# Optimization experiments

Measured on AMD Instinct MI355X. Metric: run time of the kernel, lower is better.

Reference implementation:

```python
import jax, jax.numpy as jnp
import numpy as np

B, N, NP, K, C_IN, C, H = 16, 4096, 1024, 32, 128, 256, 4
C_G = C_IN + 3  # grouped feature dim (use_xyz concat of relative coords)
EPS = 1e-3      # keras LayerNormalization default epsilon


def setup_inputs() -> dict:
    key = jax.random.key(0)
    ks = jax.random.split(key, 16)
    s = 0.05
    return {
        "xyz": jax.random.normal(ks[0], (B, N, 3), jnp.float32),
        "newxyz": jax.random.normal(ks[1], (B, NP, 3), jnp.float32),
        "feature_input": jax.random.normal(ks[2], (B, N, C_IN), jnp.float32),
        "w_qkv": jax.random.normal(ks[3], (C_G, 3 * C), jnp.float32) * s,
        "proj_w": jax.random.normal(ks[4], (C, C), jnp.float32) * s,
        "proj_b": jnp.zeros((C,), jnp.float32),
        "dense_w": jax.random.normal(ks[5], (C_G, C), jnp.float32) * s,
        "dense_b": jnp.zeros((C,), jnp.float32),
        "fc1_w": jax.random.normal(ks[6], (C, 2 * C), jnp.float32) * s,
        "fc1_b": jnp.zeros((2 * C,), jnp.float32),
        "fc2_w": jax.random.normal(ks[7], (2 * C, C), jnp.float32) * s,
        "fc2_b": jnp.zeros((C,), jnp.float32),
        "n1_g": jnp.ones((C_G,), jnp.float32),
        "n1_b": jnp.zeros((C_G,), jnp.float32),
        "n2_g": jnp.ones((C,), jnp.float32),
        "n2_b": jnp.zeros((C,), jnp.float32),
        "group_num": K,
        "training": True,
    }


def _layernorm(x, g, b):
    m = jnp.mean(x, axis=-1, keepdims=True)
    v = jnp.mean(jnp.square(x - m), axis=-1, keepdims=True)
    return (x - m) * jax.lax.rsqrt(v + EPS) * g + b


def _sample_and_group(newxyz, group_num, xyz, feats):
    # squared pairwise distances (B, NP, N)
    d2 = (jnp.sum(newxyz**2, -1)[:, :, None]
          - 2.0 * jnp.einsum('bpc,bnc->bpn', newxyz, xyz)
          + jnp.sum(xyz**2, -1)[:, None, :])
    _, idx = jax.lax.top_k(-d2, group_num)            # (B, NP, K) nearest
    b_idx = jnp.arange(newxyz.shape[0])[:, None, None]
    grouped_xyz = xyz[b_idx, idx] - newxyz[:, :, None, :]   # (B, NP, K, 3)
    grouped_feat = feats[b_idx, idx]                        # (B, NP, K, C_IN)
    return jnp.concatenate([grouped_xyz, grouped_feat], axis=-1)


def _self_attention(x, w_qkv, proj_w, proj_b):
    b, n, k = x.shape[0], x.shape[1], x.shape[2]
    d = C // H
    qkv = jnp.einsum('bnkc,cd->bnkd', x, w_qkv)
    qkv = qkv.reshape(b, n, k, 3, H, d)
    qkv = jnp.transpose(qkv, (3, 0, 1, 4, 2, 5))      # (3, B, NP, H, K, d)
    q, kk, v = qkv[0], qkv[1], qkv[2]
    qm = jnp.max(q, axis=-2, keepdims=True)           # (B, NP, H, 1, d)
    attn = jnp.einsum('bnhqd,bnhkd->bnhqk', qm, kk) * (C ** -0.5)
    attn = jax.nn.softmax(attn, axis=-1)
    out = jnp.einsum('bnhqk,bnhkd->bnhqd', attn, v)[..., 0, :]  # (B, NP, H, d)
    out = out.reshape(b, n, C)
    return jax.nn.relu(out @ proj_w + proj_b)


def reference(xyz, newxyz, feature_input, w_qkv, proj_w, proj_b, dense_w,
              dense_b, fc1_w, fc1_b, fc2_w, fc2_b, n1_g, n1_b, n2_g, n2_b,
              group_num, training):
    gf = _sample_and_group(newxyz, group_num, xyz, feature_input)  # (B,NP,K,C_G)
    feat = _self_attention(_layernorm(gf, n1_g, n1_b), w_qkv, proj_w, proj_b)
    feat = feat + jax.nn.relu(jnp.max(gf, axis=-2) @ dense_w + dense_b)
    f2 = _layernorm(feat, n2_g, n2_b)
    f2 = jax.nn.relu(f2 @ fc1_w + fc1_b)
    f2 = f2 @ fc2_w + fc2_b
    return f2 + feat
```

## Files before the change

kernel.cpp:

```cpp
#include <hip/hip_runtime.h>
#include <hip/hip_bf16.h>

typedef __hip_bfloat16 bf16;

#define Bn   16
#define Nn   4096
#define NPn  1024
#define Kn   32
#define CINn 128
#define CGn  131
#define Cn   256
#define Hn   4
#define KPAD 160
#define XBS  168
#define XFS2 136
#define GFS  136

typedef __attribute__((ext_vector_type(8))) short frag_ab;
typedef __attribute__((ext_vector_type(4))) float frag_cd;

__device__ __forceinline__ float b2f(bf16 x) { return __bfloat162float(x); }
__device__ __forceinline__ bf16  f2b(float x) { return __float2bfloat16(x); }
__device__ __forceinline__ short f2bs(float x) {
  union { bf16 h; short s; } u; u.h = __float2bfloat16(x); return u.s;
}
__device__ __forceinline__ float bs2f(short s) {
  union { short v; bf16 h; } u; u.v = s; return __bfloat162float(u.h);
}
__device__ __forceinline__ unsigned f2ord(float f) {
  unsigned u = __float_as_uint(f);
  return u ^ ((u >> 31) ? 0xffffffffu : 0x80000000u);
}

__global__ __launch_bounds__(256) void knn_kernel(const float* __restrict__ xyz,
                                                  const float* __restrict__ newxyz,
                                                  int* __restrict__ idx_out) {
  constexpr int CAP = 2048;
  __shared__ unsigned long long tmin[256];
  __shared__ __align__(16) unsigned long long cand[CAP + 4];
  __shared__ unsigned long long wtau[4];
  __shared__ unsigned long long wred[4];
  __shared__ int scnt;
  const int bp  = blockIdx.x;
  const int b   = bp >> 10;
  const int tid = threadIdx.x;
  const float qx = newxyz[bp*3 + 0];
  const float qy = newxyz[bp*3 + 1];
  const float qz = newxyz[bp*3 + 2];
  const float sn = __fadd_rn(__fadd_rn(__fmul_rn(qx,qx), __fmul_rn(qy,qy)),
                             __fmul_rn(qz,qz));
  const float* xb = xyz + (size_t)b * Nn * 3;
  unsigned long long key[16];
  unsigned long long lmin = ~0ull;
  #pragma unroll
  for (int s = 0; s < 16; ++s) {
    const int n = s*256 + tid;
    const float xx = xb[n*3 + 0];
    const float xy = xb[n*3 + 1];
    const float xz = xb[n*3 + 2];
    const float sx  = __fadd_rn(__fadd_rn(__fmul_rn(xx,xx), __fmul_rn(xy,xy)),
                                __fmul_rn(xz,xz));
    const float dot = __fadd_rn(__fadd_rn(__fmul_rn(qx,xx), __fmul_rn(qy,xy)),
                                __fmul_rn(qz,xz));
    const float d2 = __fadd_rn(__fsub_rn(sn, __fmul_rn(2.0f, dot)), sx);
    key[s] = ((unsigned long long)f2ord(d2) << 32) | (unsigned)n;
    if (key[s] < lmin) lmin = key[s];
  }
  const int lane = tid & 63, wv = tid >> 6;

  if (tid == 0) scnt = 0;
  tmin[tid] = lmin;
  __syncthreads();

  {
    const unsigned long long* wt = &tmin[wv * 64];
    int rk = 0;
    #pragma unroll 8
    for (int j = 0; j < 64; ++j) rk += (wt[j] < lmin) ? 1 : 0;
    if (rk == 31) wtau[wv] = lmin;
  }
  __syncthreads();
  unsigned long long tau = wtau[0];
  if (wtau[1] < tau) tau = wtau[1];
  if (wtau[2] < tau) tau = wtau[2];
  if (wtau[3] < tau) tau = wtau[3];

  #pragma unroll
  for (int s = 0; s < 16; ++s) {
    if (key[s] <= tau) {
      const int p = atomicAdd(&scnt, 1);
      if (p < CAP) cand[p] = key[s];
    }
  }
  __syncthreads();
  const int m = scnt;

  if (m <= CAP) {
    if (tid < 4) cand[m + tid] = ~0ull;
    __syncthreads();
    const int m4 = (m + 3) & ~3;
    for (int t = tid; t < m; t += 256) {
      const unsigned long long mykey = cand[t];
      int r = 0;
      for (int j = 0; j < m4; j += 4) {
        r += (cand[j+0] < mykey) ? 1 : 0;
        r += (cand[j+1] < mykey) ? 1 : 0;
        r += (cand[j+2] < mykey) ? 1 : 0;
        r += (cand[j+3] < mykey) ? 1 : 0;
      }
      if (r < Kn) idx_out[(size_t)bp*Kn + r] = (int)(mykey & 0xffffffffu);
    }
  } else {
    for (int s = 0; s < Kn; ++s) {
      unsigned long long mm = lmin;
      #pragma unroll
      for (int d = 32; d; d >>= 1) {
        const unsigned lo = __shfl_xor((unsigned)(mm & 0xffffffffu), d, 64);
        const unsigned hi = __shfl_xor((unsigned)(mm >> 32), d, 64);
        const unsigned long long o = ((unsigned long long)hi << 32) | lo;
        if (o < mm) mm = o;
      }
      if (lane == 0) wred[wv] = mm;
      __syncthreads();
      unsigned long long best = wred[0];
      if (wred[1] < best) best = wred[1];
      if (wred[2] < best) best = wred[2];
      if (wred[3] < best) best = wred[3];
      __syncthreads();
      const int n = (int)(best & 0xffffffffu);
      if (tid == 0) idx_out[(size_t)bp*Kn + s] = n;
      if ((n & 255) == tid) {
        const int slot = n >> 8;
        #pragma unroll
        for (int t = 0; t < 16; ++t) if (t == slot) key[t] = ~0ull;
        unsigned long long m2 = ~0ull;
        #pragma unroll
        for (int t = 0; t < 16; ++t) if (key[t] < m2) m2 = key[t];
        lmin = m2;
      }
    }
  }
}

__global__ __launch_bounds__(256) void wprep_all_kernel(
    const float* __restrict__ w_qkv, const float* __restrict__ proj_w,
    const float* __restrict__ dense_w, const float* __restrict__ fc1_w,
    const float* __restrict__ fc2_w, short* __restrict__ o_qkv,
    short* __restrict__ o_proj, short* __restrict__ o_dense,
    short* __restrict__ o_fc1, short* __restrict__ o_fc2) {
  const int blk = blockIdx.x;
  const float* W; short* out; int K, N, nnt, remap, base;
  if      (blk <  480) { W=w_qkv;   out=o_qkv;   K=CGn; N=768; nnt=48; remap=1; base=0;    }
  else if (blk <  736) { W=proj_w;  out=o_proj;  K=Cn;  N=256; nnt=16; remap=0; base=480;  }
  else if (blk <  896) { W=dense_w; out=o_dense; K=CGn; N=256; nnt=16; remap=1; base=736;  }
  else if (blk < 1408) { W=fc1_w;   out=o_fc1;   K=Cn;  N=512; nnt=32; remap=0; base=896;  }
  else                 { W=fc2_w;   out=o_fc2;   K=512; N=256; nnt=16; remap=0; base=1408; }
  const int t = (blk - base) * 256 + threadIdx.x;
  const int j    = t & 7;
  const int lane = (t >> 3) & 63;
  const int nt   = (t >> 9) % nnt;
  const int kt   = (t >> 9) / nnt;
  const int k = kt*32 + (lane >> 4)*8 + j;
  const int n = nt*16 + (lane & 15);
  int krow = k;
  if (remap) krow = (k < 128) ? k + 3 : k - 128;
  out[t] = (k < K) ? f2bs(W[(size_t)krow*N + n]) : (short)0;
}

__global__ __launch_bounds__(256, 2) void fused_attn_kernel(
    const float* __restrict__ xyz, const float* __restrict__ newxyz,
    const float* __restrict__ featin, const short* __restrict__ wfrag,
    const float* __restrict__ n1g, const float* __restrict__ n1b,
    const int* __restrict__ idx, bf16* __restrict__ attnout,
    bf16* __restrict__ gfmax) {
  __shared__ __align__(16) short Xs[64 * XBS];
  __shared__ float sg[CGn], sb[CGn];
  __shared__ int sidx[64];
  const int bp0 = blockIdx.x * 2;
  const int b   = bp0 >> 10;
  const int tid = threadIdx.x;
  if (tid < 64) {
    int n = idx[(size_t)bp0*Kn + tid];
    sidx[tid] = ((unsigned)n < (unsigned)Nn) ? n : 0;
  }
  if (tid < CGn) {
    const int rj = (tid < 128) ? tid + 3 : tid - 128;
    sg[tid] = n1g[rj];
    sb[tid] = n1b[rj];
  }
  __syncthreads();
  const int kk = tid >> 3, sub = tid & 7;
  float4 r[2][4];
  float ex[2] = {0.f, 0.f};
  #pragma unroll
  for (int p = 0; p < 2; ++p) {
    const int row = p*32 + kk;
    const float* frow = featin + ((size_t)b*Nn + sidx[row])*CINn;
    #pragma unroll
    for (int i = 0; i < 4; ++i) r[p][i] = *(const float4*)(frow + sub*4 + 32*i);
    if (sub < 3)
      ex[p] = xyz[((size_t)b*Nn + sidx[row])*3 + sub] - newxyz[(bp0+p)*3 + sub];
  }
  #pragma unroll
  for (int p = 0; p < 2; ++p) {
    const int row = p*32 + kk;
    #pragma unroll
    for (int i = 0; i < 4; ++i) {
      short4 s4 = { f2bs(r[p][i].x), f2bs(r[p][i].y), f2bs(r[p][i].z), f2bs(r[p][i].w) };
      *(short4*)&Xs[row*XFS2 + sub*4 + 32*i] = s4;
    }
    if (sub < 3) Xs[row*XFS2 + 128 + sub] = f2bs(ex[p]);
  }
  float mean[2], rstd[2];
  #pragma unroll
  for (int p = 0; p < 2; ++p) {
    float s = ex[p], s2 = ex[p]*ex[p];
    #pragma unroll
    for (int i = 0; i < 4; ++i) {
      s  += r[p][i].x + r[p][i].y + r[p][i].z + r[p][i].w;
      s2 += r[p][i].x*r[p][i].x + r[p][i].y*r[p][i].y
          + r[p][i].z*r[p][i].z + r[p][i].w*r[p][i].w;
    }
    s  += __shfl_xor(s, 1, 64);  s  += __shfl_xor(s, 2, 64);  s  += __shfl_xor(s, 4, 64);
    s2 += __shfl_xor(s2, 1, 64); s2 += __shfl_xor(s2, 2, 64); s2 += __shfl_xor(s2, 4, 64);
    mean[p] = s * (1.0f/CGn);
    const float var = s2 * (1.0f/CGn) - mean[p]*mean[p];
    rstd[p] = rsqrtf(var + 1e-3f);
  }
  __syncthreads();
  #pragma unroll
  for (int p = 0; p < 2; ++p) {
    if (tid < GFS) {
      float m = 0.f;
      if (tid < CGn) {
        m = -1e30f;
        #pragma unroll
        for (int k2 = 0; k2 < Kn; ++k2)
          m = fmaxf(m, bs2f(Xs[(p*32 + k2)*XFS2 + tid]));
      }
      gfmax[(size_t)(bp0+p)*GFS + tid] = f2b(m);
    }
  }
  __syncthreads();
  #pragma unroll
  for (int p = 0; p < 2; ++p) {
    const int row = p*32 + kk;
    #pragma unroll
    for (int i = 0; i < 4; ++i) {
      const float4 g4 = *(const float4*)&sg[sub*4 + 32*i];
      const float4 b4 = *(const float4*)&sb[sub*4 + 32*i];
      short4 s4;
      s4.x = f2bs((r[p][i].x - mean[p])*rstd[p]*g4.x + b4.x);
      s4.y = f2bs((r[p][i].y - mean[p])*rstd[p]*g4.y + b4.y);
      s4.z = f2bs((r[p][i].z - mean[p])*rstd[p]*g4.z + b4.z);
      s4.w = f2bs((r[p][i].w - mean[p])*rstd[p]*g4.w + b4.w);
      *(short4*)&Xs[row*XBS + sub*4 + 32*i] = s4;
    }
    if (sub < 3)
      Xs[row*XBS + 128 + sub] = f2bs((ex[p] - mean[p])*rstd[p]*sg[128+sub] + sb[128+sub]);
  }
  #pragma unroll
  for (int u = 0; u < 8; ++u) {
    const int e = u*256 + tid;
    const int row = e >> 5, jj = 131 + (e & 31);
    if (jj < 160) Xs[row*XBS + jj] = 0;
  }
  __syncthreads();
  const int lane = tid & 63, w = tid >> 6;
  const int col = lane & 15, quad = lane >> 4;
  float qm[2][4], aw[2][2][4], inv[2];
  {
    frag_cd acc[4][4] = {};
    for (int kt = 0; kt < 5; ++kt) {
      const int ko = kt*32 + quad*8;
      frag_ab a[4];
      #pragma unroll
      for (int mt = 0; mt < 4; ++mt)
        a[mt] = *(const frag_ab*)&Xs[(mt*16 + col)*XBS + ko];
      #pragma unroll
      for (int ntl = 0; ntl < 4; ++ntl) {
        const int nt = w*4 + ntl;
        const frag_ab bfr = *(const frag_ab*)(wfrag + ((size_t)(kt*48 + nt)*64 + lane)*8);
        #pragma unroll
        for (int mt = 0; mt < 4; ++mt)
          acc[ntl][mt] = __builtin_amdgcn_mfma_f32_16x16x32_bf16(a[mt], bfr, acc[ntl][mt], 0, 0, 0);
      }
    }
    #pragma unroll
    for (int p = 0; p < 2; ++p)
      #pragma unroll
      for (int ntl = 0; ntl < 4; ++ntl) {
        float m = -1e30f;
        #pragma unroll
        for (int mtl = 0; mtl < 2; ++mtl)
          #pragma unroll
          for (int rr = 0; rr < 4; ++rr) m = fmaxf(m, acc[ntl][p*2+mtl][rr]);
        m = fmaxf(m, __shfl_xor(m, 16, 64));
        m = fmaxf(m, __shfl_xor(m, 32, 64));
        qm[p][ntl] = m;
      }
  }
  {
    frag_cd acc[4][4] = {};
    for (int kt = 0; kt < 5; ++kt) {
      const int ko = kt*32 + quad*8;
      frag_ab a[4];
      #pragma unroll
      for (int mt = 0; mt < 4; ++mt)
        a[mt] = *(const frag_ab*)&Xs[(mt*16 + col)*XBS + ko];
      #pragma unroll
      for (int ntl = 0; ntl < 4; ++ntl) {
        const int nt = 16 + w*4 + ntl;
        const frag_ab bfr = *(const frag_ab*)(wfrag + ((size_t)(kt*48 + nt)*64 + lane)*8);
        #pragma unroll
        for (int mt = 0; mt < 4; ++mt)
          acc[ntl][mt] = __builtin_amdgcn_mfma_f32_16x16x32_bf16(a[mt], bfr, acc[ntl][mt], 0, 0, 0);
      }
    }
    #pragma unroll
    for (int p = 0; p < 2; ++p) {
      float lg[2][4];
      #pragma unroll
      for (int mtl = 0; mtl < 2; ++mtl)
        #pragma unroll
        for (int rr = 0; rr < 4; ++rr) {
          float pp = 0.f;
          #pragma unroll
          for (int ntl = 0; ntl < 4; ++ntl) pp = fmaf(qm[p][ntl], acc[ntl][p*2+mtl][rr], pp);
          #pragma unroll
          for (int d = 1; d < 16; d <<= 1) pp += __shfl_xor(pp, d, 64);
          lg[mtl][rr] = pp * 0.0625f;
        }
      float mx = -1e30f;
      #pragma unroll
      for (int mtl = 0; mtl < 2; ++mtl)
        #pragma unroll
        for (int rr = 0; rr < 4; ++rr) mx = fmaxf(mx, lg[mtl][rr]);
      mx = fmaxf(mx, __shfl_xor(mx, 16, 64));
      mx = fmaxf(mx, __shfl_xor(mx, 32, 64));
      float ssum = 0.f;
      #pragma unroll
      for (int mtl = 0; mtl < 2; ++mtl)
        #pragma unroll
        for (int rr = 0; rr < 4; ++rr) { aw[p][mtl][rr] = expf(lg[mtl][rr] - mx); ssum += aw[p][mtl][rr]; }
      ssum += __shfl_xor(ssum, 16, 64);
      ssum += __shfl_xor(ssum, 32, 64);
      inv[p] = 1.f / ssum;
    }
  }
  {
    frag_cd acc[4][4] = {};
    for (int kt = 0; kt < 5; ++kt) {
      const int ko = kt*32 + quad*8;
      frag_ab a[4];
      #pragma unroll
      for (int mt = 0; mt < 4; ++mt)
        a[mt] = *(const frag_ab*)&Xs[(mt*16 + col)*XBS + ko];
      #pragma unroll
      for (int ntl = 0; ntl < 4; ++ntl) {
        const int nt = 32 + w*4 + ntl;
        const frag_ab bfr = *(const frag_ab*)(wfrag + ((size_t)(kt*48 + nt)*64 + lane)*8);
        #pragma unroll
        for (int mt = 0; mt < 4; ++mt)
          acc[ntl][mt] = __builtin_amdgcn_mfma_f32_16x16x32_bf16(a[mt], bfr, acc[ntl][mt], 0, 0, 0);
      }
    }
    #pragma unroll
    for (int p = 0; p < 2; ++p)
      #pragma unroll
      for (int ntl = 0; ntl < 4; ++ntl) {
        float o = 0.f;
        #pragma unroll
        for (int mtl = 0; mtl < 2; ++mtl)
          #pragma unroll
          for (int rr = 0; rr < 4; ++rr) o = fmaf(aw[p][mtl][rr], acc[ntl][p*2+mtl][rr], o);
        o += __shfl_xor(o, 16, 64);
        o += __shfl_xor(o, 32, 64);
        if (quad == 0)
          attnout[(size_t)(bp0+p)*Cn + w*64 + ntl*16 + col] = f2b(o * inv[p]);
      }
  }
}

template<bool RELU, bool ADD_S, bool OUT_BF16>
__global__ __launch_bounds__(256) void mfma_gemm_kernel(
    const bf16* __restrict__ A, int lda, int Ka,
    const short* __restrict__ Wf, int nnt_total, int N,
    const float* __restrict__ bias, const bf16* __restrict__ S,
    void* __restrict__ Dv) {
  __shared__ __align__(16) short As[64*40];
  const int m0 = blockIdx.y * 64;
  const int n0 = blockIdx.x * 128;
  const int tid = threadIdx.x, lane = tid & 63, w = tid >> 6;
  const int col = lane & 15, quad = lane >> 4;
  const int row = tid >> 2, c8 = (tid & 3) * 8;
  frag_cd acc[4][2] = {};
  const int nkt = (Ka + 31) >> 5;
  for (int kt = 0; kt < nkt; ++kt) {
    const int k0 = kt*32 + c8;
    frag_ab av = {0,0,0,0,0,0,0,0};
    if (k0 + 8 <= Ka)
      av = *(const frag_ab*)((const short*)A + (size_t)(m0+row)*lda + k0);
    __syncthreads();
    *(frag_ab*)&As[row*40 + c8] = av;
    __syncthreads();
    frag_ab afr[4];
    #pragma unroll
    for (int mt = 0; mt < 4; ++mt)
      afr[mt] = *(const frag_ab*)&As[(mt*16 + col)*40 + quad*8];
    #pragma unroll
    for (int ntl = 0; ntl < 2; ++ntl) {
      const int nt = (n0 >> 4) + w*2 + ntl;
      const frag_ab bfr = *(const frag_ab*)(Wf + ((size_t)(kt*nnt_total + nt)*64 + lane)*8);
      #pragma unroll
      for (int mt = 0; mt < 4; ++mt)
        acc[mt][ntl] = __builtin_amdgcn_mfma_f32_16x16x32_bf16(afr[mt], bfr, acc[mt][ntl], 0, 0, 0);
    }
  }
  #pragma unroll
  for (int ntl = 0; ntl < 2; ++ntl) {
    const int n = n0 + w*32 + ntl*16 + col;
    const float bv = bias[n];
    #pragma unroll
    for (int mt = 0; mt < 4; ++mt) {
      #pragma unroll
      for (int r = 0; r < 4; ++r) {
        const int m = m0 + mt*16 + quad*4 + r;
        float v = acc[mt][ntl][r] + bv;
        if (RELU) v = fmaxf(v, 0.f);
        if (ADD_S) v += b2f(S[(size_t)m*N + n]);
        if (OUT_BF16) ((bf16*)Dv)[(size_t)m*N + n] = f2b(v);
        else          ((float*)Dv)[(size_t)m*N + n] = v;
      }
    }
  }
}

__global__ __launch_bounds__(256) void dual_gemm_kernel(
    const bf16* __restrict__ A1, const short* __restrict__ W1,
    const bf16* __restrict__ A2, const short* __restrict__ W2,
    const float* __restrict__ b1, const float* __restrict__ b2,
    bf16* __restrict__ D) {
  __shared__ __align__(16) short As[64*40];
  const int m0 = blockIdx.y * 64;
  const int n0 = blockIdx.x * 128;
  const int tid = threadIdx.x, lane = tid & 63, w = tid >> 6;
  const int col = lane & 15, quad = lane >> 4;
  const int row = tid >> 2, c8 = (tid & 3) * 8;
  frag_cd acc1[4][2] = {}, acc2[4][2] = {};
  for (int kt = 0; kt < 8; ++kt) {
    const frag_ab av = *(const frag_ab*)((const short*)A1 + (size_t)(m0+row)*Cn + kt*32 + c8);
    __syncthreads();
    *(frag_ab*)&As[row*40 + c8] = av;
    __syncthreads();
    frag_ab afr[4];
    #pragma unroll
    for (int mt = 0; mt < 4; ++mt)
      afr[mt] = *(const frag_ab*)&As[(mt*16 + col)*40 + quad*8];
    #pragma unroll
    for (int ntl = 0; ntl < 2; ++ntl) {
      const int nt = (n0 >> 4) + w*2 + ntl;
      const frag_ab bfr = *(const frag_ab*)(W1 + ((size_t)(kt*16 + nt)*64 + lane)*8);
      #pragma unroll
      for (int mt = 0; mt < 4; ++mt)
        acc1[mt][ntl] = __builtin_amdgcn_mfma_f32_16x16x32_bf16(afr[mt], bfr, acc1[mt][ntl], 0, 0, 0);
    }
  }
  for (int kt = 0; kt < 5; ++kt) {
    const int k0 = kt*32 + c8;
    frag_ab av = {0,0,0,0,0,0,0,0};
    if (k0 + 8 <= GFS)
      av = *(const frag_ab*)((const short*)A2 + (size_t)(m0+row)*GFS + k0);
    __syncthreads();
    *(frag_ab*)&As[row*40 + c8] = av;
    __syncthreads();
    frag_ab afr[4];
    #pragma unroll
    for (int mt = 0; mt < 4; ++mt)
      afr[mt] = *(const frag_ab*)&As[(mt*16 + col)*40 + quad*8];
    #pragma unroll
    for (int ntl = 0; ntl < 2; ++ntl) {
      const int nt = (n0 >> 4) + w*2 + ntl;
      const frag_ab bfr = *(const frag_ab*)(W2 + ((size_t)(kt*16 + nt)*64 + lane)*8);
      #pragma unroll
      for (int mt = 0; mt < 4; ++mt)
        acc2[mt][ntl] = __builtin_amdgcn_mfma_f32_16x16x32_bf16(afr[mt], bfr, acc2[mt][ntl], 0, 0, 0);
    }
  }
  #pragma unroll
  for (int ntl = 0; ntl < 2; ++ntl) {
    const int n = n0 + w*32 + ntl*16 + col;
    const float bv1 = b1[n], bv2 = b2[n];
    #pragma unroll
    for (int mt = 0; mt < 4; ++mt) {
      #pragma unroll
      for (int r = 0; r < 4; ++r) {
        const int m = m0 + mt*16 + quad*4 + r;
        const float v = fmaxf(acc1[mt][ntl][r] + bv1, 0.f)
                      + fmaxf(acc2[mt][ntl][r] + bv2, 0.f);
        D[(size_t)m*Cn + n] = f2b(v);
      }
    }
  }
}

__global__ __launch_bounds__(256) void ln2_kernel(const bf16* __restrict__ feat,
                                                  const float* __restrict__ g,
                                                  const float* __restrict__ b,
                                                  bf16* __restrict__ out) {
  const int r = blockIdx.x*4 + (threadIdx.x >> 6), lane = threadIdx.x & 63;
  float vv[4];
  #pragma unroll
  for (int c = 0; c < 4; ++c) vv[c] = b2f(feat[(size_t)r*Cn + lane*4 + c]);
  float s  = vv[0] + vv[1] + vv[2] + vv[3];
  float s2 = vv[0]*vv[0] + vv[1]*vv[1] + vv[2]*vv[2] + vv[3]*vv[3];
  #pragma unroll
  for (int d = 32; d; d >>= 1) { s += __shfl_xor(s, d, 64); s2 += __shfl_xor(s2, d, 64); }
  const float mean = s * (1.f/256.f);
  const float var  = s2 * (1.f/256.f) - mean*mean;
  const float rstd = rsqrtf(var + 1e-3f);
  #pragma unroll
  for (int c = 0; c < 4; ++c) {
    const int cc = lane*4 + c;
    out[(size_t)r*Cn + cc] = f2b((vv[c] - mean)*rstd*g[cc] + b[cc]);
  }
}

extern "C" void kernel_launch(void* const* d_in, const int* in_sizes, int n_in,
                              void* d_out, int out_size, void* d_ws, size_t ws_size,
                              hipStream_t stream) {
  const float* xyz     = (const float*)d_in[0];
  const float* newxyz  = (const float*)d_in[1];
  const float* featin  = (const float*)d_in[2];
  const float* w_qkv   = (const float*)d_in[3];
  const float* proj_w  = (const float*)d_in[4];
  const float* proj_b  = (const float*)d_in[5];
  const float* dense_w = (const float*)d_in[6];
  const float* dense_b = (const float*)d_in[7];
  const float* fc1_w   = (const float*)d_in[8];
  const float* fc1_b   = (const float*)d_in[9];
  const float* fc2_w   = (const float*)d_in[10];
  const float* fc2_b   = (const float*)d_in[11];
  const float* n1g     = (const float*)d_in[12];
  const float* n1b     = (const float*)d_in[13];
  const float* n2g     = (const float*)d_in[14];
  const float* n2b     = (const float*)d_in[15];

  char*  ws     = (char*)d_ws;
  short* wqkv   = (short*)(ws + 0);
  short* wproj  = (short*)(ws + 245760);
  short* wdense = (short*)(ws + 376832);
  short* wfc1   = (short*)(ws + 458752);
  short* wfc2   = (short*)(ws + 720896);
  bf16*  featB  = (bf16*)(ws + 1048576);
  bf16*  attnA  = (bf16*)(ws + 9437184);
  bf16*  gfmax  = (bf16*)(ws + 17825792);
  int*   idxws  = (int*) (ws + 22282240);
  bf16*  fc1out = (bf16*)(ws + 24379392);

  const int M = Bn * NPn;

  knn_kernel<<<dim3(M), dim3(256), 0, stream>>>(xyz, newxyz, idxws);
  wprep_all_kernel<<<dim3(1920), dim3(256), 0, stream>>>(
      w_qkv, proj_w, dense_w, fc1_w, fc2_w, wqkv, wproj, wdense, wfc1, wfc2);

  fused_attn_kernel<<<dim3(M/2), dim3(256), 0, stream>>>(
      xyz, newxyz, featin, wqkv, n1g, n1b, idxws, attnA, gfmax);
  dual_gemm_kernel<<<dim3(2, M/64), dim3(256), 0, stream>>>(
      attnA, wproj, gfmax, wdense, proj_b, dense_b, featB);
  ln2_kernel<<<dim3(M/4), dim3(256), 0, stream>>>(featB, n2g, n2b, attnA);
  mfma_gemm_kernel<true, false, true><<<dim3(4, M/64), dim3(256), 0, stream>>>(
      attnA, Cn, Cn, wfc1, 32, 512, fc1_b, (const bf16*)nullptr, fc1out);
  mfma_gemm_kernel<false, true, false><<<dim3(2, M/64), dim3(256), 0, stream>>>(
      fc1out, 512, 512, wfc2, 16, Cn, fc2_b, featB, d_out);
}
```

Baseline: 482.5 us.

## Precompute xyz norms, tighten KNN threshold, one query point per attention block

A new prep kernel packs xyz with its squared norm into float4, so the KNN kernel does one vector load per point instead of three scalar loads plus the norm arithmetic. The KNN candidate threshold moves from the rank-31 to the rank-15 per-wave minimum, which cuts the candidate count and the quadratic ranking work. A fallback path handles the case where fewer than K candidates survive. The fused attention kernel now handles one query point per block instead of two, halving LDS and register use to allow 4 blocks per CU, at the cost of twice as many blocks and repeated weight-fragment loads.

Measured after the change: 447.9 us. 7.2% less time.

```diff
diff --git a/kernel.cpp b/kernel.cpp
--- a/kernel.cpp
+++ b/kernel.cpp
@@ -32,7 +32,18 @@
   return u ^ ((u >> 31) ? 0xffffffffu : 0x80000000u);
 }
 
-__global__ __launch_bounds__(256) void knn_kernel(const float* __restrict__ xyz,
+__global__ __launch_bounds__(256) void xyzw_prep_kernel(
+    const float* __restrict__ xyz, float4* __restrict__ xyzw) {
+  const int i = blockIdx.x * 256 + threadIdx.x;
+  const float x = xyz[i*3 + 0];
+  const float y = xyz[i*3 + 1];
+  const float z = xyz[i*3 + 2];
+  const float sx = __fadd_rn(__fadd_rn(__fmul_rn(x,x), __fmul_rn(y,y)),
+                             __fmul_rn(z,z));
+  xyzw[i] = make_float4(x, y, z, sx);
+}
+
+__global__ __launch_bounds__(256) void knn_kernel(const float4* __restrict__ xyzw,
                                                   const float* __restrict__ newxyz,
                                                   int* __restrict__ idx_out) {
   constexpr int CAP = 2048;
@@ -49,20 +60,16 @@
   const float qz = newxyz[bp*3 + 2];
   const float sn = __fadd_rn(__fadd_rn(__fmul_rn(qx,qx), __fmul_rn(qy,qy)),
                              __fmul_rn(qz,qz));
-  const float* xb = xyz + (size_t)b * Nn * 3;
+  const float4* xb = xyzw + (size_t)b * Nn;
   unsigned long long key[16];
   unsigned long long lmin = ~0ull;
   #pragma unroll
   for (int s = 0; s < 16; ++s) {
     const int n = s*256 + tid;
-    const float xx = xb[n*3 + 0];
-    const float xy = xb[n*3 + 1];
-    const float xz = xb[n*3 + 2];
-    const float sx  = __fadd_rn(__fadd_rn(__fmul_rn(xx,xx), __fmul_rn(xy,xy)),
-                                __fmul_rn(xz,xz));
-    const float dot = __fadd_rn(__fadd_rn(__fmul_rn(qx,xx), __fmul_rn(qy,xy)),
-                                __fmul_rn(qz,xz));
-    const float d2 = __fadd_rn(__fsub_rn(sn, __fmul_rn(2.0f, dot)), sx);
+    const float4 xw = xb[n];
+    const float dot = __fadd_rn(__fadd_rn(__fmul_rn(qx,xw.x), __fmul_rn(qy,xw.y)),
+                                __fmul_rn(qz,xw.z));
+    const float d2 = __fadd_rn(__fsub_rn(sn, __fmul_rn(2.0f, dot)), xw.w);
     key[s] = ((unsigned long long)f2ord(d2) << 32) | (unsigned)n;
     if (key[s] < lmin) lmin = key[s];
   }
@@ -77,7 +84,7 @@
     int rk = 0;
     #pragma unroll 8
     for (int j = 0; j < 64; ++j) rk += (wt[j] < lmin) ? 1 : 0;
-    if (rk == 31) wtau[wv] = lmin;
+    if (rk == 15) wtau[wv] = lmin;
   }
   __syncthreads();
   unsigned long long tau = wtau[0];
@@ -95,7 +102,7 @@
   __syncthreads();
   const int m = scnt;
 
-  if (m <= CAP) {
+  if (m >= Kn && m <= CAP) {
     if (tid < 4) cand[m + tid] = ~0ull;
     __syncthreads();
     const int m4 = (m + 3) & ~3;
@@ -167,20 +174,20 @@
   out[t] = (k < K) ? f2bs(W[(size_t)krow*N + n]) : (short)0;
 }
 
-__global__ __launch_bounds__(256, 2) void fused_attn_kernel(
+__global__ __launch_bounds__(256, 4) void fused_attn_kernel(
     const float* __restrict__ xyz, const float* __restrict__ newxyz,
     const float* __restrict__ featin, const short* __restrict__ wfrag,
     const float* __restrict__ n1g, const float* __restrict__ n1b,
     const int* __restrict__ idx, bf16* __restrict__ attnout,
     bf16* __restrict__ gfmax) {
-  __shared__ __align__(16) short Xs[64 * XBS];
+  __shared__ __align__(16) short Xs[32 * XBS];
   __shared__ float sg[CGn], sb[CGn];
-  __shared__ int sidx[64];
-  const int bp0 = blockIdx.x * 2;
-  const int b   = bp0 >> 10;
+  __shared__ int sidx[32];
+  const int bp  = blockIdx.x;
+  const int b   = bp >> 10;
   const int tid = threadIdx.x;
-  if (tid < 64) {
-    int n = idx[(size_t)bp0*Kn + tid];
+  if (tid < 32) {
+    int n = idx[(size_t)bp*Kn + tid];
     sidx[tid] = ((unsigned)n < (unsigned)Nn) ? n : 0;
   }
   if (tid < CGn) {
@@ -190,77 +197,62 @@
   }
   __syncthreads();
   const int kk = tid >> 3, sub = tid & 7;
-  float4 r[2][4];
-  float ex[2] = {0.f, 0.f};
-  #pragma unroll
-  for (int p = 0; p < 2; ++p) {
-    const int row = p*32 + kk;
-    const float* frow = featin + ((size_t)b*Nn + sidx[row])*CINn;
-    #pragma unroll
-    for (int i = 0; i < 4; ++i) r[p][i] = *(const float4*)(frow + sub*4 + 32*i);
+  float4 r[4];
+  float ex = 0.f;
+  {
+    const float* frow = featin + ((size_t)b*Nn + sidx[kk])*CINn;
+    #pragma unroll
+    for (int i = 0; i < 4; ++i) r[i] = *(const float4*)(frow + sub*4 + 32*i);
     if (sub < 3)
-      ex[p] = xyz[((size_t)b*Nn + sidx[row])*3 + sub] - newxyz[(bp0+p)*3 + sub];
-  }
-  #pragma unroll
-  for (int p = 0; p < 2; ++p) {
-    const int row = p*32 + kk;
+      ex = xyz[((size_t)b*Nn + sidx[kk])*3 + sub] - newxyz[bp*3 + sub];
+  }
+  #pragma unroll
+  for (int i = 0; i < 4; ++i) {
+    short4 s4 = { f2bs(r[i].x), f2bs(r[i].y), f2bs(r[i].z), f2bs(r[i].w) };
+    *(short4*)&Xs[kk*XFS2 + sub*4 + 32*i] = s4;
+  }
+  if (sub < 3) Xs[kk*XFS2 + 128 + sub] = f2bs(ex);
+  float mean, rstd;
+  {
+    float s = ex, s2 = ex*ex;
     #pragma unroll
     for (int i = 0; i < 4; ++i) {
-      short4 s4 = { f2bs(r[p][i].x), f2bs(r[p][i].y), f2bs(r[p][i].z), f2bs(r[p][i].w) };
-      *(short4*)&Xs[row*XFS2 + sub*4 + 32*i] = s4;
-    }
-    if (sub < 3) Xs[row*XFS2 + 128 + sub] = f2bs(ex[p]);
-  }
-  float mean[2], rstd[2];
-  #pragma unroll
-  for (int p = 0; p < 2; ++p) {
-    float s = ex[p], s2 = ex[p]*ex[p];
-    #pragma unroll
-    for (int i = 0; i < 4; ++i) {
-      s  += r[p][i].x + r[p][i].y + r[p][i].z + r[p][i].w;
-      s2 += r[p][i].x*r[p][i].x + r[p][i].y*r[p][i].y
-          + r[p][i].z*r[p][i].z + r[p][i].w*r[p][i].w;
+      s  += r[i].x + r[i].y + r[i].z + r[i].w;
+      s2 += r[i].x*r[i].x + r[i].y*r[i].y + r[i].z*r[i].z + r[i].w*r[i].w;
     }
     s  += __shfl_xor(s, 1, 64);  s  += __shfl_xor(s, 2, 64);  s  += __shfl_xor(s, 4, 64);
     s2 += __shfl_xor(s2, 1, 64); s2 += __shfl_xor(s2, 2, 64); s2 += __shfl_xor(s2, 4, 64);
-    mean[p] = s * (1.0f/CGn);
-    const float var = s2 * (1.0f/CGn) - mean[p]*mean[p];
-    rstd[p] = rsqrtf(var + 1e-3f);
-  }
-  __syncthreads();
-  #pragma unroll
-  for (int p = 0; p < 2; ++p) {
-    if (tid < GFS) {
-      float m = 0.f;
-      if (tid < CGn) {
-        m = -1e30f;
-        #pragma unroll
-        for (int k2 = 0; k2 < Kn; ++k2)
-          m = fmaxf(m, bs2f(Xs[(p*32 + k2)*XFS2 + tid]));
-      }
-      gfmax[(size_t)(bp0+p)*GFS + tid] = f2b(m);
-    }
-  }
-  __syncthreads();
-  #pragma unroll
-  for (int p = 0; p < 2; ++p) {
-    const int row = p*32 + kk;
-    #pragma unroll
-    for (int i = 0; i < 4; ++i) {
-      const float4 g4 = *(const float4*)&sg[sub*4 + 32*i];
-      const float4 b4 = *(const float4*)&sb[sub*4 + 32*i];
-      short4 s4;
-      s4.x = f2bs((r[p][i].x - mean[p])*rstd[p]*g4.x + b4.x);
-      s4.y = f2bs((r[p][i].y - mean[p])*rstd[p]*g4.y + b4.y);
-      s4.z = f2bs((r[p][i].z - mean[p])*rstd[p]*g4.z + b4.z);
-      s4.w = f2bs((r[p][i].w - mean[p])*rstd[p]*g4.w + b4.w);
-      *(short4*)&Xs[row*XBS + sub*4 + 32*i] = s4;
-    }
-    if (sub < 3)
-      Xs[row*XBS + 128 + sub] = f2bs((ex[p] - mean[p])*rstd[p]*sg[128+sub] + sb[128+sub]);
-  }
-  #pragma unroll
-  for (int u = 0; u < 8; ++u) {
+    mean = s * (1.0f/CGn);
+    const float var = s2 * (1.0f/CGn) - mean*mean;
+    rstd = rsqrtf(var + 1e-3f);
+  }
+  __syncthreads();
+  if (tid < GFS) {
+    float m = 0.f;
+    if (tid < CGn) {
+      m = -1e30f;
+      #pragma unroll
+      for (int k2 = 0; k2 < Kn; ++k2)
+        m = fmaxf(m, bs2f(Xs[k2*XFS2 + tid]));
+    }
+    gfmax[(size_t)bp*GFS + tid] = f2b(m);
+  }
+  __syncthreads();
+  #pragma unroll
+  for (int i = 0; i < 4; ++i) {
+    const float4 g4 = *(const float4*)&sg[sub*4 + 32*i];
+    const float4 b4 = *(const float4*)&sb[sub*4 + 32*i];
+    short4 s4;
+    s4.x = f2bs((r[i].x - mean)*rstd*g4.x + b4.x);
+    s4.y = f2bs((r[i].y - mean)*rstd*g4.y + b4.y);
+    s4.z = f2bs((r[i].z - mean)*rstd*g4.z + b4.z);
+    s4.w = f2bs((r[i].w - mean)*rstd*g4.w + b4.w);
+    *(short4*)&Xs[kk*XBS + sub*4 + 32*i] = s4;
+  }
+  if (sub < 3)
+    Xs[kk*XBS + 128 + sub] = f2bs((ex - mean)*rstd*sg[128+sub] + sb[128+sub]);
+  #pragma unroll
+  for (int u = 0; u < 4; ++u) {
     const int e = u*256 + tid;
     const int row = e >> 5, jj = 131 + (e & 31);
     if (jj < 160) Xs[row*XBS + jj] = 0;
@@ -268,117 +260,110 @@
   __syncthreads();
   const int lane = tid & 63, w = tid >> 6;
   const int col = lane & 15, quad = lane >> 4;
-  float qm[2][4], aw[2][2][4], inv[2];
+  float qm[4], aw[2][4], inv;
   {
-    frag_cd acc[4][4] = {};
+    frag_cd acc[4][2] = {};
     for (int kt = 0; kt < 5; ++kt) {
       const int ko = kt*32 + quad*8;
-      frag_ab a[4];
-      #pragma unroll
-      for (int mt = 0; mt < 4; ++mt)
+      frag_ab a[2];
+      #pragma unroll
+      for (int mt = 0; mt < 2; ++mt)
         a[mt] = *(const frag_ab*)&Xs[(mt*16 + col)*XBS + ko];
       #pragma unroll
       for (int ntl = 0; ntl < 4; ++ntl) {
         const int nt = w*4 + ntl;
         const frag_ab bfr = *(const frag_ab*)(wfrag + ((size_t)(kt*48 + nt)*64 + lane)*8);
         #pragma unroll
-        for (int mt = 0; mt < 4; ++mt)
+        for (int mt = 0; mt < 2; ++mt)
           acc[ntl][mt] = __builtin_amdgcn_mfma_f32_16x16x32_bf16(a[mt], bfr, acc[ntl][mt], 0, 0, 0);
       }
     }
     #pragma unroll
-    for (int p = 0; p < 2; ++p)
-      #pragma unroll
-      for (int ntl = 0; ntl < 4; ++ntl) {
-        float m = -1e30f;
-        #pragma unroll
-        for (int mtl = 0; mtl < 2; ++mtl)
-          #pragma unroll
-          for (int rr = 0; rr < 4; ++rr) m = fmaxf(m, acc[ntl][p*2+mtl][rr]);
-        m = fmaxf(m, __shfl_xor(m, 16, 64));
-        m = fmaxf(m, __shfl_xor(m, 32, 64));
-        qm[p][ntl] = m;
-      }
+    for (int ntl = 0; ntl < 4; ++ntl) {
+      float m = -1e30f;
+      #pragma unroll
+      for (int mt = 0; mt < 2; ++mt)
+        #pragma unroll
+        for (int rr = 0; rr < 4; ++rr) m = fmaxf(m, acc[ntl][mt][rr]);
+      m = fmaxf(m, __shfl_xor(m, 16, 64));
+      m = fmaxf(m, __shfl_xor(m, 32, 64));
+      qm[ntl] = m;
+    }
   }
   {
-    frag_cd acc[4][4] = {};
+    frag_cd acc[4][2] = {};
     for (int kt = 0; kt < 5; ++kt) {
       const int ko = kt*32 + quad*8;
-      frag_ab a[4];
-      #pragma unroll
-      for (int mt = 0; mt < 4; ++mt)
+      frag_ab a[2];
+      #pragma unroll
+      for (int mt = 0; mt < 2; ++mt)
         a[mt] = *(const frag_ab*)&Xs[(mt*16 + col)*XBS + ko];
       #pragma unroll
       for (int ntl = 0; ntl < 4; ++ntl) {
         const int nt = 16 + w*4 + ntl;
         const frag_ab bfr = *(const frag_ab*)(wfrag + ((size_t)(kt*48 + nt)*64 + lane)*8);
         #pragma unroll
-        for (int mt = 0; mt < 4; ++mt)
+        for (int mt = 0; mt < 2; ++mt)
           acc[ntl][mt] = __builtin_amdgcn_mfma_f32_16x16x32_bf16(a[mt], bfr, acc[ntl][mt], 0, 0, 0);
       }
     }
-    #pragma unroll
-    for (int p = 0; p < 2; ++p) {
-      float lg[2][4];
-      #pragma unroll
-      for (int mtl = 0; mtl < 2; ++mtl)
-        #pragma unroll
-        for (int rr = 0; rr < 4; ++rr) {
-          float pp = 0.f;
-          #pragma unroll
-          for (int ntl = 0; ntl < 4; ++ntl) pp = fmaf(qm[p][ntl], acc[ntl][p*2+mtl][rr], pp);
-          #pragma unroll
-          for (int d = 1; d < 16; d <<= 1) pp += __shfl_xor(pp, d, 64);
-          lg[mtl][rr] = pp * 0.0625f;
-        }
-      float mx = -1e30f;
-      #pragma unroll
-      for (int mtl = 0; mtl < 2; ++mtl)
-        #pragma unroll
-        for (int rr = 0; rr < 4; ++rr) mx = fmaxf(mx, lg[mtl][rr]);
-      mx = fmaxf(mx, __shfl_xor(mx, 16, 64));
-      mx = fmaxf(mx, __shfl_xor(mx, 32, 64));
-      float ssum = 0.f;
-      #pragma unroll
-      for (int mtl = 0; mtl < 2; ++mtl)
-        #pragma unroll
-        for (int rr = 0; rr < 4; ++rr) { aw[p][mtl][rr] = expf(lg[mtl][rr] - mx); ssum += aw[p][mtl][rr]; }
-      ssum += __shfl_xor(ssum, 16, 64);
-      ssum += __shfl_xor(ssum, 32, 64);
-      inv[p] = 1.f / ssum;
-    }
+    float lg[2][4];
+    #pragma unroll
+    for (int mtl = 0; mtl < 2; ++mtl)
+      #pragma unroll
+      for (int rr = 0; rr < 4; ++rr) {
+        float pp = 0.f;
+        #pragma unroll
+        for (int ntl = 0; ntl < 4; ++ntl) pp = fmaf(qm[ntl], acc[ntl][mtl][rr], pp);
+        #pragma unroll
+        for (int d = 1; d < 16; d <<= 1) pp += __shfl_xor(pp, d, 64);
+        lg[mtl][rr] = pp * 0.0625f;
+      }
+    float mx = -1e30f;
+    #pragma unroll
+    for (int mtl = 0; mtl < 2; ++mtl)
+      #pragma unroll
+      for (int rr = 0; rr < 4; ++rr) mx = fmaxf(mx, lg[mtl][rr]);
+    mx = fmaxf(mx, __shfl_xor(mx, 16, 64));
+    mx = fmaxf(mx, __shfl_xor(mx, 32, 64));
+    float ssum = 0.f;
+    #pragma unroll
+    for (int mtl = 0; mtl < 2; ++mtl)
+      #pragma unroll
+      for (int rr = 0; rr < 4; ++rr) { aw[mtl][rr] = expf(lg[mtl][rr] - mx); ssum += aw[mtl][rr]; }
+    ssum += __shfl_xor(ssum, 16, 64);
+    ssum += __shfl_xor(ssum, 32, 64);
+    inv = 1.f / ssum;
   }
   {
-    frag_cd acc[4][4] = {};
+    frag_cd acc[4][2] = {};
     for (int kt = 0; kt < 5; ++kt) {
       const int ko = kt*32 + quad*8;
-      frag_ab a[4];
-      #pragma unroll
-      for (int mt = 0; mt < 4; ++mt)
+      frag_ab a[2];
+      #pragma unroll
+      for (int mt = 0; mt < 2; ++mt)
         a[mt] = *(const frag_ab*)&Xs[(mt*16 + col)*XBS + ko];
       #pragma unroll
       for (int ntl = 0; ntl < 4; ++ntl) {
         const int nt = 32 + w*4 + ntl;
         const frag_ab bfr = *(const frag_ab*)(wfrag + ((size_t)(kt*48 + nt)*64 + lane)*8);
         #pragma unroll
-        for (int mt = 0; mt < 4; ++mt)
+        for (int mt = 0; mt < 2; ++mt)
           acc[ntl][mt] = __builtin_amdgcn_mfma_f32_16x16x32_bf16(a[mt], bfr, acc[ntl][mt], 0, 0, 0);
       }
     }
     #pragma unroll
-    for (int p = 0; p < 2; ++p)
-      #pragma unroll
-      for (int ntl = 0; ntl < 4; ++ntl) {
-        float o = 0.f;
-        #pragma unroll
-        for (int mtl = 0; mtl < 2; ++mtl)
-          #pragma unroll
-          for (int rr = 0; rr < 4; ++rr) o = fmaf(aw[p][mtl][rr], acc[ntl][p*2+mtl][rr], o);
-        o += __shfl_xor(o, 16, 64);
-        o += __shfl_xor(o, 32, 64);
-        if (quad == 0)
-          attnout[(size_t)(bp0+p)*Cn + w*64 + ntl*16 + col] = f2b(o * inv[p]);
-      }
+    for (int ntl = 0; ntl < 4; ++ntl) {
+      float o = 0.f;
+      #pragma unroll
+      for (int mtl = 0; mtl < 2; ++mtl)
+        #pragma unroll
+        for (int rr = 0; rr < 4; ++rr) o = fmaf(aw[mtl][rr], acc[ntl][mtl][rr], o);
+      o += __shfl_xor(o, 16, 64);
+      o += __shfl_xor(o, 32, 64);
+      if (quad == 0)
+        attnout[(size_t)bp*Cn + w*64 + ntl*16 + col] = f2b(o * inv);
+    }
   }
 }
 
@@ -557,14 +542,16 @@
   bf16*  gfmax  = (bf16*)(ws + 17825792);
   int*   idxws  = (int*) (ws + 22282240);
   bf16*  fc1out = (bf16*)(ws + 24379392);
+  float4* xyzw  = (float4*)(ws + 24379392);
 
   const int M = Bn * NPn;
 
-  knn_kernel<<<dim3(M), dim3(256), 0, stream>>>(xyz, newxyz, idxws);
+  xyzw_prep_kernel<<<dim3(Bn*Nn/256), dim3(256), 0, stream>>>(xyz, xyzw);
+  knn_kernel<<<dim3(M), dim3(256), 0, stream>>>(xyzw, newxyz, idxws);
   wprep_all_kernel<<<dim3(1920), dim3(256), 0, stream>>>(
       w_qkv, proj_w, dense_w, fc1_w, fc2_w, wqkv, wproj, wdense, wfc1, wfc2);
 
-  fused_attn_kernel<<<dim3(M/2), dim3(256), 0, stream>>>(
+  fused_attn_kernel<<<dim3(M), dim3(256), 0, stream>>>(
       xyz, newxyz, featin, wqkv, n1g, n1b, idxws, attnA, gfmax);
   dual_gemm_kernel<<<dim3(2, M/64), dim3(256), 0, stream>>>(
       attnA, wproj, gfmax, wdense, proj_b, dense_b, featB);
```
